# Kernel optimization log

Hardware: AMD Instinct MI355X
Metric: run time of the kernel (lower is better)

Reference implementation:

```python
import jax, jax.numpy as jnp
import numpy as np

B, T, E, H, V = 128, 64, 512, 1024, 10000


def setup_inputs() -> dict:
    key = jax.random.key(0)
    ks = jax.random.split(key, 9)
    s = 0.05
    return {
        "features": jax.random.normal(ks[0], (B, E), dtype=jnp.float32),
        "captions": jax.random.randint(ks[1], (B, T), 0, V, dtype=jnp.int64),
        "embed_W": jax.random.normal(ks[2], (V, E), dtype=jnp.float32) * s,
        "W_ih": jax.random.normal(ks[3], (4 * H, E), dtype=jnp.float32) * s,
        "W_hh": jax.random.normal(ks[4], (4 * H, H), dtype=jnp.float32) * s,
        "b_ih": jax.random.normal(ks[5], (4 * H,), dtype=jnp.float32) * s,
        "b_hh": jax.random.normal(ks[6], (4 * H,), dtype=jnp.float32) * s,
        "fc_W": jax.random.normal(ks[7], (V, H), dtype=jnp.float32) * s,
        "fc_b": jax.random.normal(ks[8], (V,), dtype=jnp.float32) * s,
    }


def reference(features, captions, embed_W, W_ih, W_hh, b_ih, b_hh, fc_W, fc_b):
    # Embed captions: [B, T, E]
    cap_emb = embed_W[captions]
    # Input sequence per the original loop: t=0 -> features, t>=1 -> cap_emb[:, t]
    xs = jnp.concatenate([features[:, None, :], cap_emb[:, 1:, :]], axis=1)  # [B, T, E]
    hdim = W_hh.shape[1]
    # Precompute input contribution to gates for all steps: [T, B, 4H]
    x_gates = jnp.einsum("bte,ge->tbg", xs, W_ih) + b_ih + b_hh

    def step(carry, xg):
        h, c = carry
        g = xg + h @ W_hh.T  # [B, 4H]
        i, f, gg, o = jnp.split(g, 4, axis=-1)
        i = jax.nn.sigmoid(i)
        f = jax.nn.sigmoid(f)
        gg = jnp.tanh(gg)
        o = jax.nn.sigmoid(o)
        c = f * c + i * gg
        h = o * jnp.tanh(c)
        return (h, c), h

    bsz = features.shape[0]
    h0 = jnp.zeros((bsz, hdim), dtype=features.dtype)
    c0 = jnp.zeros((bsz, hdim), dtype=features.dtype)
    _, hs = jax.lax.scan(step, (h0, c0), x_gates)  # hs: [T, B, H]
    # Output projection per step: [B, T, V]
    out = jnp.einsum("tbh,vh->btv", hs, fc_W) + fc_b
    return out
```

## Files before the change

### kernel.cpp

```cpp
#include <hip/hip_runtime.h>
#include <math.h>

static constexpr int Bb = 128;
static constexpr int Tt = 64;
static constexpr int Ee = 512;
static constexpr int Hh = 1024;
static constexpr int Vv = 10000;
static constexpr int G  = 4 * Hh;
static constexpr int Vpad = 10240;

typedef __attribute__((ext_vector_type(8))) short short8;
typedef __attribute__((ext_vector_type(4))) float floatx4;

__device__ __forceinline__ unsigned short f2bf(float f) {
    unsigned u = __float_as_uint(f);
    return (unsigned short)((u + 0x7fffu + ((u >> 16) & 1u)) >> 16);
}
__device__ __forceinline__ float bf2f(unsigned short u) {
    return __uint_as_float((unsigned)u << 16);
}

__device__ __forceinline__ void gload16(const void* g, void* l) {
    __builtin_amdgcn_global_load_lds(
        (const __attribute__((address_space(1))) void*)g,
        (__attribute__((address_space(3))) void*)l, 16, 0, 0);
}

__device__ __forceinline__ void store_nt(float* p, float v) {
    asm volatile("global_store_dword %0, %1, off nt"
                 :: "v"((unsigned long long)(uintptr_t)p), "v"(v) : "memory");
}

__device__ __forceinline__ float sigmoid_fast(float x) {
    return __builtin_amdgcn_rcpf(1.f + __expf(-x));
}
__device__ __forceinline__ float tanh_fast(float x) {
    float e = __expf(-2.f * fabsf(x));
    float t = (1.f - e) * __builtin_amdgcn_rcpf(1.f + e);
    return copysignf(t, x);
}

__device__ __forceinline__ void cvt8_body(const float* __restrict__ s,
                                          unsigned short* __restrict__ d,
                                          int n, int i8) {
    short8 v;
    #pragma unroll
    for (int j = 0; j < 8; ++j) {
        int e = i8 + j;
        float f = (e < n) ? s[e] : 0.f;
        v[j] = (short)f2bf(f);
    }
    *reinterpret_cast<short8*>(d + i8) = v;
}

__global__ __launch_bounds__(256)
void prep(const float* __restrict__ W_ih, const float* __restrict__ W_hh,
          const float* __restrict__ fc_W, const float* __restrict__ features,
          const int* __restrict__ captions, const float* __restrict__ embed_W,
          unsigned short* __restrict__ wihb, unsigned short* __restrict__ whhb,
          unsigned short* __restrict__ fcwb, unsigned short* __restrict__ xsb) {
    const int blk = blockIdx.x;
    const int tid = threadIdx.x;
    if (blk < 1024) {
        cvt8_body(W_ih, wihb, G * Ee, (blk * 256 + tid) * 8);
    } else if (blk < 3072) {
        cvt8_body(W_hh, whhb, G * Hh, ((blk - 1024) * 256 + tid) * 8);
    } else if (blk < 8192) {
        cvt8_body(fc_W, fcwb, Vv * Hh, ((blk - 3072) * 256 + tid) * 8);
    } else {
        int idx = (blk - 8192) * 256 + tid;
        int m  = idx >> 6;
        int c8 = (idx & 63) * 8;
        int t = m >> 7;
        int b = m & 127;
        const float* src;
        if (t == 0) {
            src = features + (size_t)b * Ee + c8;
        } else {
            int tok = captions[(size_t)b * Tt + t];
            src = embed_W + (size_t)tok * Ee + c8;
        }
        short8 v;
        #pragma unroll
        for (int j = 0; j < 8; ++j) v[j] = (short)f2bf(src[j]);
        *reinterpret_cast<short8*>(xsb + (size_t)m * Ee + c8) = v;
    }
}

__device__ __forceinline__ void stage_half(
    const unsigned short* __restrict__ Gsrc, int Kdim, int rowbase, int k0,
    unsigned short* ldsbase, int tid) {
    int e = tid * 16;
    int r = e >> 6;
    int c = e & 63;
    int c_log = c ^ (((r >> 1) & 3) << 4);
    gload16(Gsrc + (size_t)(rowbase + r) * Kdim + k0 + (c_log >> 1),
            ldsbase + tid * 8);
}

template<int MODE>
__global__ __launch_bounds__(512, 2)
void gemm256(const unsigned short* __restrict__ A,
             const unsigned short* __restrict__ Bm,
             int M, int N, int K,
             const float* __restrict__ bias0, const float* __restrict__ bias1,
             void* __restrict__ Cv) {
    constexpr int BK = 32;
    __shared__ unsigned short lds[4 * 2 * 256 * BK];

    const int nwg = gridDim.x * gridDim.y;
    const int flat = blockIdx.y * gridDim.x + blockIdx.x;
    const int tix = (flat & 7) * (nwg >> 3) + (flat >> 3);
    const int bx = tix % gridDim.x;
    const int by = tix / gridDim.x;

    const int tid  = threadIdx.x;
    const int wid  = tid >> 6;
    const int lane = tid & 63;
    const int wm = wid >> 2;
    const int wn = wid & 3;
    const int row0 = bx * 256;
    const int col0 = by * 256;
    const int l15 = lane & 15;
    const int kq  = lane >> 4;

    const int NT = K / BK;

    const int swz = (kq ^ ((l15 >> 1) & 3)) * 8;
    const int arow_s = wm * 4096 + l15 * 32 + swz;
    const int brow_s = 8192 + (wn >> 1) * 4096 + ((wn & 1) * 64 + l15) * 32 + swz;

    floatx4 acc[8][4];
    #pragma unroll
    for (int i = 0; i < 8; ++i)
        #pragma unroll
        for (int j = 0; j < 4; ++j) acc[i][j] = (floatx4)0.f;

    stage_half(A,  K, row0,       0,  &lds[0],     tid);
    stage_half(A,  K, row0 + 128, 0,  &lds[4096],  tid);
    stage_half(Bm, K, col0,       0,  &lds[8192],  tid);
    stage_half(Bm, K, col0 + 128, 0,  &lds[12288], tid);
    stage_half(A,  K, row0,       BK, &lds[16384 + 0],     tid);
    stage_half(A,  K, row0 + 128, BK, &lds[16384 + 4096],  tid);
    stage_half(Bm, K, col0,       BK, &lds[16384 + 8192],  tid);
    stage_half(Bm, K, col0 + 128, BK, &lds[16384 + 12288], tid);
    asm volatile("s_waitcnt vmcnt(4)" ::: "memory");
    asm volatile("s_barrier" ::: "memory");

    for (int t = 0; t < NT; ++t) {
        const int cur = (t & 3) * 16384;
        short8 af[8], bfr[4];
        #pragma unroll
        for (int fi = 0; fi < 8; ++fi)
            af[fi] = *reinterpret_cast<const short8*>(&lds[cur + arow_s + fi * 512]);
        #pragma unroll
        for (int fj = 0; fj < 4; ++fj)
            bfr[fj] = *reinterpret_cast<const short8*>(&lds[cur + brow_s + fj * 512]);
        if (t + 2 < NT) {
            const int nb = ((t + 2) & 3) * 16384;
            stage_half(A,  K, row0,       (t + 2) * BK, &lds[nb],         tid);
            stage_half(A,  K, row0 + 128, (t + 2) * BK, &lds[nb + 4096],  tid);
            stage_half(Bm, K, col0,       (t + 2) * BK, &lds[nb + 8192],  tid);
            stage_half(Bm, K, col0 + 128, (t + 2) * BK, &lds[nb + 12288], tid);
        }
        __builtin_amdgcn_s_setprio(1);
        #pragma unroll
        for (int fi = 0; fi < 8; ++fi)
            #pragma unroll
            for (int fj = 0; fj < 4; ++fj)
                acc[fi][fj] = __builtin_amdgcn_mfma_f32_16x16x32_bf16(
                    af[fi], bfr[fj], acc[fi][fj], 0, 0, 0);
        __builtin_amdgcn_s_setprio(0);
        if (t + 1 < NT) {
            if (t + 2 < NT) asm volatile("s_waitcnt vmcnt(4)" ::: "memory");
            else            asm volatile("s_waitcnt vmcnt(0)" ::: "memory");
            asm volatile("s_barrier" ::: "memory");
        }
    }

    if (MODE == 1) {
        unsigned short* C = (unsigned short*)Cv;
        #pragma unroll
        for (int fi = 0; fi < 8; ++fi)
            #pragma unroll
            for (int fj = 0; fj < 4; ++fj)
                #pragma unroll
                for (int q = 0; q < 4; ++q) {
                    int m = row0 + wm * 128 + fi * 16 + kq * 4 + q;
                    int n = col0 + wn * 64 + fj * 16 + l15;
                    C[(size_t)m * N + n] =
                        f2bf(acc[fi][fj][q] + bias0[n] + bias1[n]);
                }
    } else {
        float* C = (float*)Cv;
        if (col0 + 256 <= N) {
            #pragma unroll
            for (int fi = 0; fi < 8; ++fi)
                #pragma unroll
                for (int fj = 0; fj < 4; ++fj)
                    #pragma unroll
                    for (int q = 0; q < 4; ++q) {
                        int m = row0 + wm * 128 + fi * 16 + kq * 4 + q;
                        int n = col0 + wn * 64 + fj * 16 + l15;
                        int t = m >> 7, b = m & 127;
                        store_nt(&C[(size_t)b * (Tt * Vv) + (size_t)t * Vv + n],
                                 acc[fi][fj][q] + bias0[n]);
                    }
        } else {
            #pragma unroll
            for (int fi = 0; fi < 8; ++fi)
                #pragma unroll
                for (int fj = 0; fj < 4; ++fj)
                    #pragma unroll
                    for (int q = 0; q < 4; ++q) {
                        int m = row0 + wm * 128 + fi * 16 + kq * 4 + q;
                        int n = col0 + wn * 64 + fj * 16 + l15;
                        if (n < N) {
                            int t = m >> 7, b = m & 127;
                            store_nt(&C[(size_t)b * (Tt * Vv)
                                        + (size_t)t * Vv + n],
                                     acc[fi][fj][q] + bias0[n]);
                        }
                    }
        }
    }
}

template<int ROT>
__device__ __forceinline__ void gate_mfma(
    const unsigned short* __restrict__ hprev,
    const short8 (&wreg)[8][4],
    int row0, int wave, int l15, int kq,
    floatx4 (&acc)[2][4])
{
    const short8* ar0 = reinterpret_cast<const short8*>(
        hprev + (size_t)(row0 + l15) * Hh) + wave * 32 + kq;
    const short8* ar1 = reinterpret_cast<const short8*>(
        hprev + (size_t)(row0 + 16 + l15) * Hh) + wave * 32 + kq;
    short8 a0[8], a1[8];
    #pragma unroll
    for (int ks = 0; ks < 8; ++ks) {
        const int j = (ks + ROT) & 7;
        a0[ks] = ar0[j * 4];
        a1[ks] = ar1[j * 4];
    }
    #pragma unroll
    for (int ks = 0; ks < 8; ++ks) {
        const int j = (ks + ROT) & 7;
        acc[0][0] = __builtin_amdgcn_mfma_f32_16x16x32_bf16(
            a0[ks], wreg[j][0], acc[0][0], 0, 0, 0);
        acc[0][1] = __builtin_amdgcn_mfma_f32_16x16x32_bf16(
            a0[ks], wreg[j][1], acc[0][1], 0, 0, 0);
        acc[0][2] = __builtin_amdgcn_mfma_f32_16x16x32_bf16(
            a0[ks], wreg[j][2], acc[0][2], 0, 0, 0);
        acc[0][3] = __builtin_amdgcn_mfma_f32_16x16x32_bf16(
            a0[ks], wreg[j][3], acc[0][3], 0, 0, 0);
    }
    #pragma unroll
    for (int ks = 0; ks < 8; ++ks) {
        const int j = (ks + ROT) & 7;
        acc[1][0] = __builtin_amdgcn_mfma_f32_16x16x32_bf16(
            a1[ks], wreg[j][0], acc[1][0], 0, 0, 0);
        acc[1][1] = __builtin_amdgcn_mfma_f32_16x16x32_bf16(
            a1[ks], wreg[j][1], acc[1][1], 0, 0, 0);
        acc[1][2] = __builtin_amdgcn_mfma_f32_16x16x32_bf16(
            a1[ks], wreg[j][2], acc[1][2], 0, 0, 0);
        acc[1][3] = __builtin_amdgcn_mfma_f32_16x16x32_bf16(
            a1[ks], wreg[j][3], acc[1][3], 0, 0, 0);
    }
}

__global__ __launch_bounds__(256, 1)
void lstm_persist(const unsigned short* __restrict__ whhb,
                  const unsigned short* __restrict__ xg,
                  unsigned short* __restrict__ hsb,
                  unsigned* __restrict__ flags) {
    __shared__ float redsum[8 * 3 * 4 * 64];
    const int tid  = threadIdx.x;
    const int w    = blockIdx.x;
    const int wg_m = w & 3;
    const int wg_n = w >> 2;
    const int wave = tid >> 6;
    const int lane = tid & 63;
    const int l15  = lane & 15;
    const int kq   = lane >> 4;

    const int row0 = wg_m * 32;
    const int hcol = wg_n * 16 + l15;
    const int lrA = (wave >> 1) * 16 + kq * 4 + ((wave & 1) * 2);
    const int lrB = lrA + 1;
    const int rotsel = (wg_n >> 1) & 3;
    unsigned* myctr = flags + (size_t)(wg_m * 8 + (wg_n >> 3)) * 16;
    float cell0 = 0.f, cell1 = 0.f;

    short8 wreg[8][4];
    {
        const unsigned short* wbase = whhb
            + (size_t)(wg_n * 16 + l15) * Hh + wave * 256 + kq * 8;
        #pragma unroll
        for (int nb = 0; nb < 4; ++nb)
            #pragma unroll
            for (int j = 0; j < 8; ++j)
                wreg[j][nb] = *reinterpret_cast<const short8*>(
                    wbase + (size_t)nb * Hh * Hh + j * 32);
    }

    float xa[2][4], xb[2][4];
    {
        const unsigned short* xr = xg + (size_t)(row0 + lrA) * G
                                 + wg_n * 16 + l15;
        #pragma unroll
        for (int nb = 0; nb < 4; ++nb) {
            xa[0][nb] = bf2f(xr[nb * Hh]);
            xa[1][nb] = bf2f(xr[G + nb * Hh]);
        }
    }

#define WRC(W_, C_)                                                            \
    if (((C_) >> 1) != (W_)) {                                                 \
        _Pragma("unroll")                                                      \
        for (int nb = 0; nb < 4; ++nb)                                         \
            redsum[((C_) * 3 + (((W_) > ((C_) >> 1)) ? (W_)-1 : (W_))) * 256   \
                   + nb * 64 + lane] = acc[(C_) >> 2][nb][(C_) & 3];           \
    }

#define SPILL(W_)                                                              \
    do {                                                                       \
        _Pragma("unroll")                                                      \
        for (int nb = 0; nb < 4; ++nb) {                                       \
            own0[nb] = acc[(2 * (W_)) >> 2][nb][(2 * (W_)) & 3];               \
            own1[nb] = acc[(2 * (W_) + 1) >> 2][nb][(2 * (W_) + 1) & 3];       \
        }                                                                      \
        WRC(W_, 0); WRC(W_, 1); WRC(W_, 2); WRC(W_, 3);                        \
        WRC(W_, 4); WRC(W_, 5); WRC(W_, 6); WRC(W_, 7);                        \
    } while (0)

#define LSTM_STEP(T, XC, XN)                                                   \
    do {                                                                       \
        const int t_ = (T);                                                    \
        floatx4 acc[2][4];                                                     \
        _Pragma("unroll")                                                      \
        for (int i = 0; i < 2; ++i)                                            \
            _Pragma("unroll")                                                  \
            for (int j = 0; j < 4; ++j) acc[i][j] = (floatx4)0.f;              \
        if (t_ > 0) {                                                          \
            if (tid < 8) {                                                     \
                const unsigned* fl = flags + (size_t)(wg_m * 8 + tid) * 16;    \
                unsigned need = 8u * (unsigned)t_;                             \
                while (__hip_atomic_load(fl, __ATOMIC_RELAXED,                 \
                                         __HIP_MEMORY_SCOPE_AGENT) < need)     \
                    __builtin_amdgcn_s_sleep(1);                               \
            }                                                                  \
            __syncthreads();                                                   \
            asm volatile("" ::: "memory");                                     \
            const unsigned short* hprev = hsb + (size_t)(t_ - 1) * (Bb * Hh);  \
            if (rotsel == 0)                                                   \
                gate_mfma<0>(hprev, wreg, row0, wave, l15, kq, acc);           \
            else if (rotsel == 1)                                              \
                gate_mfma<2>(hprev, wreg, row0, wave, l15, kq, acc);           \
            else if (rotsel == 2)                                              \
                gate_mfma<4>(hprev, wreg, row0, wave, l15, kq, acc);           \
            else                                                               \
                gate_mfma<6>(hprev, wreg, row0, wave, l15, kq, acc);           \
        }                                                                      \
        float own0[4], own1[4];                                                \
        if (wave == 0)      SPILL(0);                                          \
        else if (wave == 1) SPILL(1);                                          \
        else if (wave == 2) SPILL(2);                                          \
        else                SPILL(3);                                          \
        __syncthreads();                                                       \
        float gA[4], gB[4];                                                    \
        {                                                                      \
            const int cA = wave * 2;                                           \
            _Pragma("unroll")                                                  \
            for (int nb = 0; nb < 4; ++nb) {                                   \
                int bA = (cA * 3) * 256 + nb * 64 + lane;                      \
                gA[nb] = own0[nb] + redsum[bA] + redsum[bA + 256]              \
                       + redsum[bA + 512] + XC[0][nb];                         \
                int bB = ((cA + 1) * 3) * 256 + nb * 64 + lane;                \
                gB[nb] = own1[nb] + redsum[bB] + redsum[bB + 256]              \
                       + redsum[bB + 512] + XC[1][nb];                         \
            }                                                                  \
        }                                                                      \
        unsigned short* ht = hsb + (size_t)t_ * (Bb * Hh);                     \
        {                                                                      \
            float si = sigmoid_fast(gA[0]);                                    \
            float sf = sigmoid_fast(gA[1]);                                    \
            float tg = tanh_fast(gA[2]);                                       \
            float so = sigmoid_fast(gA[3]);                                    \
            float cn = sf * cell0 + si * tg;                                   \
            cell0 = cn;                                                        \
            float h = so * tanh_fast(cn);                                      \
            __hip_atomic_store(&ht[(size_t)(row0 + lrA) * Hh + hcol], f2bf(h), \
                               __ATOMIC_RELAXED, __HIP_MEMORY_SCOPE_AGENT);    \
        }                                                                      \
        {                                                                      \
            float si = sigmoid_fast(gB[0]);                                    \
            float sf = sigmoid_fast(gB[1]);                                    \
            float tg = tanh_fast(gB[2]);                                       \
            float so = sigmoid_fast(gB[3]);                                    \
            float cn = sf * cell1 + si * tg;                                   \
            cell1 = cn;                                                        \
            float h = so * tanh_fast(cn);                                      \
            __hip_atomic_store(&ht[(size_t)(row0 + lrB) * Hh + hcol], f2bf(h), \
                               __ATOMIC_RELAXED, __HIP_MEMORY_SCOPE_AGENT);    \
        }                                                                      \
        __builtin_amdgcn_sched_barrier(0);                                     \
        if (t_ + 1 < Tt) {      \
            const unsigned short* xr = xg + (size_t)(t_ + 1) * (Bb * G)        \
                + (size_t)(row0 + lrA) * G + wg_n * 16 + l15;                  \
            _Pragma("unroll")                                                  \
            for (int nb = 0; nb < 4; ++nb) {                                   \
                XN[0][nb] = bf2f(xr[nb * Hh]);                                 \
                XN[1][nb] = bf2f(xr[G + nb * Hh]);                             \
            }                                                                  \
        }                                                                      \
        __builtin_amdgcn_sched_barrier(0);                                     \
        if (t_ < Tt - 1) {                                                     \
                \
            asm volatile("s_waitcnt vmcnt(8)" ::: "memory");                   \
            __builtin_amdgcn_sched_barrier(0);                                 \
            __builtin_amdgcn_s_barrier();                                      \
            __builtin_amdgcn_sched_barrier(0);                                 \
            if (tid == 0)                                                      \
                __hip_atomic_fetch_add(myctr, 1u, __ATOMIC_RELAXED,            \
                                       __HIP_MEMORY_SCOPE_AGENT);              \
        }                                                                      \
    } while (0)

    for (int tt = 0; tt < Tt; tt += 2) {
        LSTM_STEP(tt,     xa, xb);
        LSTM_STEP(tt + 1, xb, xa);
    }
#undef LSTM_STEP
#undef SPILL
#undef WRC
}

extern "C" void kernel_launch(void* const* d_in, const int* in_sizes, int n_in,
                              void* d_out, int out_size, void* d_ws, size_t ws_size,
                              hipStream_t stream) {
    const float* features = (const float*)d_in[0];
    const int*   captions = (const int*)d_in[1];
    const float* embed_W  = (const float*)d_in[2];
    const float* W_ih     = (const float*)d_in[3];
    const float* W_hh     = (const float*)d_in[4];
    const float* b_ih     = (const float*)d_in[5];
    const float* b_hh     = (const float*)d_in[6];
    const float* fc_W     = (const float*)d_in[7];
    const float* fc_b     = (const float*)d_in[8];
    float* out = (float*)d_out;

    unsigned short* xsb  = (unsigned short*)d_ws;
    unsigned short* wihb = xsb  + (size_t)Tt * Bb * Ee;
    unsigned short* whhb = wihb + (size_t)G * Ee;
    unsigned short* fcwb = whhb + (size_t)G * Hh;
    unsigned short* hsb  = fcwb + (size_t)Vpad * Hh;
    unsigned short* xgb  = hsb + (size_t)Tt * Bb * Hh;
    unsigned* flags = (unsigned*)(xgb + (size_t)Tt * Bb * G);

    (void)hipMemsetAsync(flags, 0, 128 * 32 * sizeof(unsigned), stream);

    prep<<<10240, 256, 0, stream>>>(W_ih, W_hh, fc_W, features, captions,
                                    embed_W, wihb, whhb, fcwb, xsb);

    {
        dim3 grid(8192 / 256, G / 256);
        gemm256<1><<<grid, 512, 0, stream>>>(
            xsb, wihb, 8192, G, Ee, b_ih, b_hh, (void*)xgb);
    }

    lstm_persist<<<256, 256, 0, stream>>>(whhb, xgb, hsb, flags);

    {
        dim3 grid(8192 / 256, Vpad / 256);
        gemm256<2><<<grid, 512, 0, stream>>>(
            hsb, fcwb, 8192, Vv, Hh, fc_b, nullptr, (void*)out);
    }
}
```

Before: 620.5 us.

## Fuse output projection into persistent LSTM kernel, overlapping via per-step flags

Merges the recurrent LSTM kernel and the final vocabulary projection GEMM into one launch. Extra blocks spin on the per-timestep completion counters and compute the FC projection for each finished timestep (128x128 tiles) while later recurrent steps run. The goal is to hide the large output GEMM behind the latency-bound recurrence. The trade-off is a much simpler, unpipelined GEMM than the previous 256-tile kernel. It also relies on the 256 LSTM blocks being resident before the waiting blocks occupy CUs, which risks deadlock or contention with the recurrence.

```diff
diff --git a/kernel.cpp b/kernel.cpp
--- a/kernel.cpp
+++ b/kernel.cpp
@@ -98,13 +98,12 @@
             ldsbase + tid * 8);
 }
 
-template<int MODE>
 __global__ __launch_bounds__(512, 2)
-void gemm256(const unsigned short* __restrict__ A,
-             const unsigned short* __restrict__ Bm,
-             int M, int N, int K,
-             const float* __restrict__ bias0, const float* __restrict__ bias1,
-             void* __restrict__ Cv) {
+void gemm256_xg(const unsigned short* __restrict__ A,
+                const unsigned short* __restrict__ Bm,
+                int M, int N, int K,
+                const float* __restrict__ bias0, const float* __restrict__ bias1,
+                unsigned short* __restrict__ C) {
     constexpr int BK = 32;
     __shared__ unsigned short lds[4 * 2 * 256 * BK];
 
@@ -178,52 +177,17 @@
         }
     }
 
-    if (MODE == 1) {
-        unsigned short* C = (unsigned short*)Cv;
-        #pragma unroll
-        for (int fi = 0; fi < 8; ++fi)
-            #pragma unroll
-            for (int fj = 0; fj < 4; ++fj)
-                #pragma unroll
-                for (int q = 0; q < 4; ++q) {
-                    int m = row0 + wm * 128 + fi * 16 + kq * 4 + q;
-                    int n = col0 + wn * 64 + fj * 16 + l15;
-                    C[(size_t)m * N + n] =
-                        f2bf(acc[fi][fj][q] + bias0[n] + bias1[n]);
-                }
-    } else {
-        float* C = (float*)Cv;
-        if (col0 + 256 <= N) {
-            #pragma unroll
-            for (int fi = 0; fi < 8; ++fi)
-                #pragma unroll
-                for (int fj = 0; fj < 4; ++fj)
-                    #pragma unroll
-                    for (int q = 0; q < 4; ++q) {
-                        int m = row0 + wm * 128 + fi * 16 + kq * 4 + q;
-                        int n = col0 + wn * 64 + fj * 16 + l15;
-                        int t = m >> 7, b = m & 127;
-                        store_nt(&C[(size_t)b * (Tt * Vv) + (size_t)t * Vv + n],
-                                 acc[fi][fj][q] + bias0[n]);
-                    }
-        } else {
-            #pragma unroll
-            for (int fi = 0; fi < 8; ++fi)
-                #pragma unroll
-                for (int fj = 0; fj < 4; ++fj)
-                    #pragma unroll
-                    for (int q = 0; q < 4; ++q) {
-                        int m = row0 + wm * 128 + fi * 16 + kq * 4 + q;
-                        int n = col0 + wn * 64 + fj * 16 + l15;
-                        if (n < N) {
-                            int t = m >> 7, b = m & 127;
-                            store_nt(&C[(size_t)b * (Tt * Vv)
-                                        + (size_t)t * Vv + n],
-                                     acc[fi][fj][q] + bias0[n]);
-                        }
-                    }
-        }
-    }
+    #pragma unroll
+    for (int fi = 0; fi < 8; ++fi)
+        #pragma unroll
+        for (int fj = 0; fj < 4; ++fj)
+            #pragma unroll
+            for (int q = 0; q < 4; ++q) {
+                int m = row0 + wm * 128 + fi * 16 + kq * 4 + q;
+                int n = col0 + wn * 64 + fj * 16 + l15;
+                C[(size_t)m * N + n] =
+                    f2bf(acc[fi][fj][q] + bias0[n] + bias1[n]);
+            }
 }
 
 template<int ROT>
@@ -271,50 +235,56 @@
 }
 
 __global__ __launch_bounds__(256, 1)
-void lstm_persist(const unsigned short* __restrict__ whhb,
-                  const unsigned short* __restrict__ xg,
-                  unsigned short* __restrict__ hsb,
-                  unsigned* __restrict__ flags) {
-    __shared__ float redsum[8 * 3 * 4 * 64];
-    const int tid  = threadIdx.x;
-    const int w    = blockIdx.x;
-    const int wg_m = w & 3;
-    const int wg_n = w >> 2;
-    const int wave = tid >> 6;
-    const int lane = tid & 63;
-    const int l15  = lane & 15;
-    const int kq   = lane >> 4;
-
-    const int row0 = wg_m * 32;
-    const int hcol = wg_n * 16 + l15;
-    const int lrA = (wave >> 1) * 16 + kq * 4 + ((wave & 1) * 2);
-    const int lrB = lrA + 1;
-    const int rotsel = (wg_n >> 1) & 3;
-    unsigned* myctr = flags + (size_t)(wg_m * 8 + (wg_n >> 3)) * 16;
-    float cell0 = 0.f, cell1 = 0.f;
-
-    short8 wreg[8][4];
-    {
-        const unsigned short* wbase = whhb
-            + (size_t)(wg_n * 16 + l15) * Hh + wave * 256 + kq * 8;
-        #pragma unroll
-        for (int nb = 0; nb < 4; ++nb)
-            #pragma unroll
-            for (int j = 0; j < 8; ++j)
-                wreg[j][nb] = *reinterpret_cast<const short8*>(
-                    wbase + (size_t)nb * Hh * Hh + j * 32);
-    }
-
-    float xa[2][4], xb[2][4];
-    {
-        const unsigned short* xr = xg + (size_t)(row0 + lrA) * G
-                                 + wg_n * 16 + l15;
-        #pragma unroll
-        for (int nb = 0; nb < 4; ++nb) {
-            xa[0][nb] = bf2f(xr[nb * Hh]);
-            xa[1][nb] = bf2f(xr[G + nb * Hh]);
-        }
-    }
+void lstm_fc(const unsigned short* __restrict__ whhb,
+             const unsigned short* __restrict__ xg,
+             unsigned short* __restrict__ hsb,
+             unsigned* __restrict__ flags,
+             const unsigned short* __restrict__ fcwb,
+             const float* __restrict__ fc_b,
+             float* __restrict__ out) {
+    __shared__ __align__(16) unsigned char smem[24576];
+    const int tid = threadIdx.x;
+
+    if (blockIdx.x < 256) {
+        float* redsum = (float*)smem;
+        const int w    = blockIdx.x;
+        const int wg_m = w & 3;
+        const int wg_n = w >> 2;
+        const int wave = tid >> 6;
+        const int lane = tid & 63;
+        const int l15  = lane & 15;
+        const int kq   = lane >> 4;
+
+        const int row0 = wg_m * 32;
+        const int hcol = wg_n * 16 + l15;
+        const int lrA = (wave >> 1) * 16 + kq * 4 + ((wave & 1) * 2);
+        const int lrB = lrA + 1;
+        const int rotsel = (wg_n >> 1) & 3;
+        unsigned* myctr = flags + (size_t)(wg_m * 8 + (wg_n >> 3)) * 16;
+        float cell0 = 0.f, cell1 = 0.f;
+
+        short8 wreg[8][4];
+        {
+            const unsigned short* wbase = whhb
+                + (size_t)(wg_n * 16 + l15) * Hh + wave * 256 + kq * 8;
+            #pragma unroll
+            for (int nb = 0; nb < 4; ++nb)
+                #pragma unroll
+                for (int j = 0; j < 8; ++j)
+                    wreg[j][nb] = *reinterpret_cast<const short8*>(
+                        wbase + (size_t)nb * Hh * Hh + j * 32);
+        }
+
+        float xa[2][4], xb[2][4];
+        {
+            const unsigned short* xr = xg + (size_t)(row0 + lrA) * G
+                                     + wg_n * 16 + l15;
+            #pragma unroll
+            for (int nb = 0; nb < 4; ++nb) {
+                xa[0][nb] = bf2f(xr[nb * Hh]);
+                xa[1][nb] = bf2f(xr[G + nb * Hh]);
+            }
+        }
 
 #define WRC(W_, C_)                                                            \
     if (((C_) >> 1) != (W_)) {                                                 \
@@ -417,7 +387,6 @@
         }                                                                      \
         __builtin_amdgcn_sched_barrier(0);                                     \
         if (t_ < Tt - 1) {                                                     \
-                \
             asm volatile("s_waitcnt vmcnt(8)" ::: "memory");                   \
             __builtin_amdgcn_sched_barrier(0);                                 \
             __builtin_amdgcn_s_barrier();                                      \
@@ -425,16 +394,104 @@
             if (tid == 0)                                                      \
                 __hip_atomic_fetch_add(myctr, 1u, __ATOMIC_RELAXED,            \
                                        __HIP_MEMORY_SCOPE_AGENT);              \
+        } else {                   \
+            asm volatile("s_waitcnt vmcnt(0)" ::: "memory");                   \
+            __builtin_amdgcn_sched_barrier(0);                                 \
+            __builtin_amdgcn_s_barrier();                                      \
+            __builtin_amdgcn_sched_barrier(0);                                 \
+            if (tid == 0)                                                      \
+                __hip_atomic_fetch_add(myctr, 1u, __ATOMIC_RELAXED,            \
+                                       __HIP_MEMORY_SCOPE_AGENT);              \
         }                                                                      \
     } while (0)
 
-    for (int tt = 0; tt < Tt; tt += 2) {
-        LSTM_STEP(tt,     xa, xb);
-        LSTM_STEP(tt + 1, xb, xa);
-    }
+        for (int tt = 0; tt < Tt; tt += 2) {
+            LSTM_STEP(tt,     xa, xb);
+            LSTM_STEP(tt + 1, xb, xa);
+        }
 #undef LSTM_STEP
 #undef SPILL
 #undef WRC
+    } else {
+        const int gb = blockIdx.x - 256;
+        const int bx = gb / 79;
+        const int by = gb - bx * 79;
+        if (tid < 32) {
+            const unsigned* fl = flags + (size_t)tid * 16;
+            unsigned need = 8u * (unsigned)(bx + 1);
+            while (__hip_atomic_load(fl, __ATOMIC_RELAXED,
+                                     __HIP_MEMORY_SCOPE_AGENT) < need)
+                __builtin_amdgcn_s_sleep(63);
+        }
+        __syncthreads();
+        asm volatile("" ::: "memory");
+
+        unsigned short* As = (unsigned short*)smem;
+        unsigned short* Bs = (unsigned short*)smem + 4096;
+        const int wid  = tid >> 6;
+        const int lane = tid & 63;
+        const int wr = wid >> 1, wc = wid & 1;
+        const int row0 = bx * 128;
+        const int col0 = by * 128;
+        const int l15 = lane & 15;
+        const int kq  = lane >> 4;
+
+        floatx4 acc[4][4];
+        #pragma unroll
+        for (int i = 0; i < 4; ++i)
+            #pragma unroll
+            for (int j = 0; j < 4; ++j) acc[i][j] = (floatx4)0.f;
+
+        for (int k0 = 0; k0 < Hh; k0 += 32) {
+            #pragma unroll
+            for (int i = 0; i < 2; ++i) {
+                int e = i * 2048 + tid * 8;
+                int r = e >> 5, k = e & 31;
+                gload16(hsb + (size_t)(row0 + r) * Hh + k0 + k, &As[e]);
+            }
+            #pragma unroll
+            for (int i = 0; i < 2; ++i) {
+                int e = i * 2048 + tid * 8;
+                int r = e >> 5, k = e & 31;
+                gload16(fcwb + (size_t)(col0 + r) * Hh + k0 + k, &Bs[e]);
+            }
+            __syncthreads();
+
+            short8 af[4], bfr[4];
+            #pragma unroll
+            for (int i = 0; i < 4; ++i) {
+                int r = wr * 64 + i * 16 + l15;
+                af[i] = *reinterpret_cast<const short8*>(&As[r * 32 + kq * 8]);
+            }
+            #pragma unroll
+            for (int j = 0; j < 4; ++j) {
+                int c = wc * 64 + j * 16 + l15;
+                bfr[j] = *reinterpret_cast<const short8*>(&Bs[c * 32 + kq * 8]);
+            }
+            #pragma unroll
+            for (int i = 0; i < 4; ++i)
+                #pragma unroll
+                for (int j = 0; j < 4; ++j)
+                    acc[i][j] = __builtin_amdgcn_mfma_f32_16x16x32_bf16(
+                        af[i], bfr[j], acc[i][j], 0, 0, 0);
+            __syncthreads();
+        }
+
+        #pragma unroll
+        for (int i = 0; i < 4; ++i)
+            #pragma unroll
+            for (int j = 0; j < 4; ++j)
+                #pragma unroll
+                for (int q = 0; q < 4; ++q) {
+                    int m = row0 + wr * 64 + i * 16 + kq * 4 + q;
+                    int n = col0 + wc * 64 + j * 16 + l15;
+                    if (n < Vv) {
+                        int t = m >> 7, b = m & 127;
+                        store_nt(&out[(size_t)b * (Tt * Vv) + (size_t)t * Vv + n],
+                                 acc[i][j][q] + fc_b[n]);
+                    }
+                }
+    }
 }
 
 extern "C" void kernel_launch(void* const* d_in, const int* in_sizes, int n_in,
@@ -466,15 +523,10 @@
 
     {
         dim3 grid(8192 / 256, G / 256);
-        gemm256<1><<<grid, 512, 0, stream>>>(
-            xsb, wihb, 8192, G, Ee, b_ih, b_hh, (void*)xgb);
-    }
-
-    lstm_persist<<<256, 256, 0, stream>>>(whhb, xgb, hsb, flags);
-
-    {
-        dim3 grid(8192 / 256, Vpad / 256);
-        gemm256<2><<<grid, 512, 0, stream>>>(
-            hsb, fcwb, 8192, Vv, Hh, fc_b, nullptr, (void*)out);
-    }
-}
+        gemm256_xg<<<grid, 512, 0, stream>>>(
+            xsb, wihb, 8192, G, Ee, b_ih, b_hh, xgb);
+    }
+
+    lstm_fc<<<256 + 64 * 79, 256, 0, stream>>>(
+        whhb, xgb, hsb, flags, fcwb, fc_b, out);
+}
```

Result: slower. 839.1 us (+35.2%).
